# Optimization experiments

Hardware: AMD Instinct MI355X
Metric: run time of the kernel (lower is better)

Reference implementation:

```python
import jax, jax.numpy as jnp
import numpy as np

N_HEADS = 16
N_KV_HEADS = 4
HEAD_DIM = 128
WINDOW = 512
THETA = 10000.0


def _rotate_half(t):
    h = t.shape[-1] // 2
    return jnp.concatenate([-t[..., h:], t[..., :h]], axis=-1)


def setup_inputs() -> dict:
    key = jax.random.key(0)
    ks = jax.random.split(key, 6)
    B, S, D = 1, 2048, 2048
    sd = 1.0 / np.sqrt(D)
    x = jax.random.normal(ks[0], (B, S, D), dtype=jnp.float32)
    Wq = jax.random.normal(ks[1], (D, N_HEADS * HEAD_DIM), dtype=jnp.float32) * sd
    Wk = jax.random.normal(ks[2], (D, N_KV_HEADS * HEAD_DIM), dtype=jnp.float32) * sd
    Wv = jax.random.normal(ks[3], (D, N_KV_HEADS * HEAD_DIM), dtype=jnp.float32) * sd
    Wo = jax.random.normal(ks[4], (N_HEADS * HEAD_DIM, D), dtype=jnp.float32) * sd
    lam = jnp.full((N_HEADS,), 0.1, dtype=jnp.float32)
    return {"x": x, "Wq": Wq, "Wk": Wk, "Wv": Wv, "Wo": Wo, "lam": lam}


def reference(x, Wq, Wk, Wv, Wo, lam):
    B, S, D = x.shape
    H, Hk, hd = N_HEADS, N_KV_HEADS, HEAD_DIM
    n_rep = H // Hk

    q = (x @ Wq).reshape(B, S, H, hd).transpose(0, 2, 1, 3)   # [B,H,S,hd]
    k = (x @ Wk).reshape(B, S, Hk, hd).transpose(0, 2, 1, 3)  # [B,Hk,S,hd]
    v = (x @ Wv).reshape(B, S, Hk, hd).transpose(0, 2, 1, 3)

    # RoPE (full head_dim rotation, duplicated freqs)
    inv_freq = 1.0 / (THETA ** (jnp.arange(0, hd, 2, dtype=jnp.float32) / hd))
    t = jnp.arange(S, dtype=jnp.float32)
    freqs = jnp.outer(t, inv_freq)                 # [S, hd/2]
    emb = jnp.concatenate([freqs, freqs], axis=-1)  # [S, hd]
    cos, sin = jnp.cos(emb), jnp.sin(emb)
    q = q * cos + _rotate_half(q) * sin
    k = k * cos + _rotate_half(k) * sin

    # GQA: repeat KV heads
    k = jnp.repeat(k, n_rep, axis=1)  # [B,H,S,hd]
    v = jnp.repeat(v, n_rep, axis=1)

    sub = hd // 2
    q1, q2 = q[..., :sub], q[..., sub:]
    k1, k2 = k[..., :sub], k[..., sub:]
    scale = 1.0 / np.sqrt(sub)

    attn1 = jnp.einsum("bhqd,bhkd->bhqk", q1, k1) * scale
    attn2 = jnp.einsum("bhqd,bhkd->bhqk", q2, k2) * scale

    # causal + sliding window mask
    row = jnp.arange(S)[:, None]
    col = jnp.arange(S)[None, :]
    allowed = (col <= row) & (col >= row - WINDOW + 1)  # [S,S]
    neg_inf = jnp.float32(-jnp.inf)
    attn1 = jnp.where(allowed, attn1, neg_inf)
    attn2 = jnp.where(allowed, attn2, neg_inf)

    a1 = jax.nn.softmax(attn1.astype(jnp.float32), axis=-1).astype(x.dtype)
    a2 = jax.nn.softmax(attn2.astype(jnp.float32), axis=-1).astype(x.dtype)

    diff = jax.nn.relu(a1 - lam.reshape(1, H, 1, 1) * a2)
    diff = diff / (diff.sum(axis=-1, keepdims=True) + 1e-6)

    out = jnp.einsum("bhqk,bhkd->bhqd", diff, v)       # [B,H,S,hd]
    out = out.transpose(0, 2, 1, 3).reshape(B, S, H * hd)
    return out @ Wo
```

## Files before the change

### kernel.cpp

```cpp
#include <hip/hip_runtime.h>

typedef unsigned int u32;
typedef unsigned short u16;
typedef __attribute__((ext_vector_type(4))) float f32x4;
typedef __attribute__((ext_vector_type(8))) short s16x8;

#define S_LEN 2048
#define DMODEL 2048
#define NH 16
#define NKV 4
#define HD 128
#define WIN 512
#define QSCALE 0.18033688011112042f

#define WAIT_VMCNT4 asm volatile("s_waitcnt vmcnt(4)" ::: "memory")
#define WAIT_VMCNT0 asm volatile("s_waitcnt vmcnt(0)" ::: "memory")

__device__ __forceinline__ u16 f2bf(float f) {
  union { float f; u32 u; } v; v.f = f;
  u32 r = v.u + 0x7FFFu + ((v.u >> 16) & 1u);
  return (u16)(r >> 16);
}
__device__ __forceinline__ float bf2f(u16 h) {
  union { u32 u; float f; } v; v.u = ((u32)h) << 16;
  return v.f;
}

__device__ __forceinline__ void async16(const void* g, void* l) {
  __builtin_amdgcn_global_load_lds((const __attribute__((address_space(1))) void*)g,
                                   (__attribute__((address_space(3))) void*)l, 16, 0, 0);
}

__global__ __launch_bounds__(256) void k_prep(const float* __restrict__ x, u16* __restrict__ xb,
                                              const float* __restrict__ Wq,
                                              const float* __restrict__ Wk,
                                              const float* __restrict__ Wv,
                                              const float* __restrict__ Wo,
                                              u16* __restrict__ WT, u16* __restrict__ WoT,
                                              float2* __restrict__ cs) {
  __shared__ float tile[32][33];
  const int bid = blockIdx.x;
  if (bid >= 14336) {
    int s = (bid - 14336) * 4 + (threadIdx.x >> 6);
    int d = threadIdx.x & 63;
    float invf = expf(-((float)(2 * d) / (float)HD) * logf(10000.0f));
    float fr = (float)s * invf;
    float sv, cv;
    sincosf(fr, &sv, &cv);
    cs[s * 64 + d] = make_float2(cv, sv);
    return;
  }
  if (bid < 4096) {
    int i = bid * 256 + threadIdx.x;
    float4 v = ((const float4*)x)[i];
    ushort4 o;
    o.x = f2bf(v.x); o.y = f2bf(v.y); o.z = f2bf(v.z); o.w = f2bf(v.w);
    ((ushort4*)xb)[i] = o;
    return;
  }
  const int b = bid - 4096;
  const float* src;
  u16* dst;
  int N, nt, kt;
  if (b < 4096) {
    src = Wq; dst = WT; N = 2048; nt = b & 63; kt = b >> 6;
  } else if (b < 5120) {
    int i = b - 4096;
    src = Wk; dst = WT + (size_t)2048 * 2048; N = 512; nt = i & 15; kt = i >> 4;
  } else if (b < 6144) {
    int i = b - 5120;
    src = Wv; dst = WT + (size_t)2560 * 2048; N = 512; nt = i & 15; kt = i >> 4;
  } else {
    int i = b - 6144;
    src = Wo; dst = WoT; N = 2048; nt = i & 63; kt = i >> 6;
  }
  const int tx = threadIdx.x & 31, ty = threadIdx.x >> 5;
  const int n0 = nt * 32, k0 = kt * 32;
#pragma unroll
  for (int i = 0; i < 4; ++i)
    tile[ty + 8 * i][tx] = src[(size_t)(k0 + ty + 8 * i) * N + n0 + tx];
  __syncthreads();
#pragma unroll
  for (int i = 0; i < 4; ++i)
    dst[(size_t)(n0 + ty + 8 * i) * 2048 + k0 + tx] = f2bf(tile[tx][ty + 8 * i]);
}

__global__ void k_rope_k(u16* __restrict__ kr, const float2* __restrict__ cs) {
  int i = blockIdx.x * blockDim.x + threadIdx.x;
  int rowg = i >> 6, d = i & 63;
  int s = rowg & (S_LEN - 1);
  float2 c = cs[s * 64 + d];
  u16* p = kr + (size_t)rowg * HD;
  float a = bf2f(p[d]), b = bf2f(p[d + 64]);
  p[d]      = f2bf(a * c.x - b * c.y);
  p[d + 64] = f2bf(b * c.x + a * c.y);
}


template <int MODE>
__global__ __launch_bounds__(256) void k_gemm(const u16* __restrict__ A, const u16* __restrict__ BT,
                                              float* __restrict__ Cf, int K, int N,
                                              u16* __restrict__ qr, u16* __restrict__ kr,
                                              u16* __restrict__ vt) {
  __shared__ u16 S[2][192 * 64];
  const int t = threadIdx.x;
  const int l = t & 63, w = t >> 6;
  const int lg = l >> 4, ll = l & 15;

  const u32 nwg = gridDim.x * gridDim.y;
  const u32 bid = blockIdx.y * gridDim.x + blockIdx.x;
  const u32 sid = (bid & 7u) * (nwg >> 3) + (bid >> 3);
  const int m0 = (int)(sid % gridDim.x) * 64;
  const int n0 = (int)(sid / gridDim.x) * 128;

  const int wm = (w >> 1) * 32, wn = (w & 1) * 64;

  const u16* gp[6];
  u32 lo[6];
#pragma unroll
  for (int j = 0; j < 6; ++j) {
    u32 u = (u32)t * 16u + (u32)j * 4096u;
    u32 row = u >> 7;
    u32 slot = ((u >> 4) & 7u) ^ (row & 7u);
    lo[j] = u;
    gp[j] = (row < 64 ? A + (size_t)(m0 + (int)row) * K
                      : BT + (size_t)(n0 + (int)(row - 64)) * K) + slot * 8;
  }
  auto stage = [&](int b, int k0) {
#pragma unroll
    for (int j = 0; j < 6; ++j) async16(gp[j] + k0, (char*)S[b] + lo[j]);
  };

  f32x4 acc[2][4];
#pragma unroll
  for (int i = 0; i < 2; ++i)
#pragma unroll
    for (int j = 0; j < 4; ++j) acc[i][j] = (f32x4){0.f, 0.f, 0.f, 0.f};

  stage(0, 0);
  __syncthreads();

  const int nit = K / 64;
#pragma unroll 2
  for (int it = 0; it < nit; ++it) {
    const int cur = it & 1;
    if (it + 1 < nit) stage(cur ^ 1, (it + 1) * 64);

    s16x8 af[2][2], bq[4][2];
#pragma unroll
    for (int mt = 0; mt < 2; ++mt) {
      u32 r = (u32)(wm + mt * 16 + ll);
#pragma unroll
      for (int ks = 0; ks < 2; ++ks)
        af[mt][ks] = *(const s16x8*)((const char*)S[cur] + r * 128u +
                                     ((((u32)(ks * 4 + lg)) ^ (r & 7u)) * 16u));
    }
#pragma unroll
    for (int nt = 0; nt < 4; ++nt) {
      u32 r = (u32)(64 + wn + nt * 16 + ll);
#pragma unroll
      for (int ks = 0; ks < 2; ++ks)
        bq[nt][ks] = *(const s16x8*)((const char*)S[cur] + r * 128u +
                                     ((((u32)(ks * 4 + lg)) ^ (r & 7u)) * 16u));
    }
#pragma unroll
    for (int ks = 0; ks < 2; ++ks)
#pragma unroll
      for (int mt = 0; mt < 2; ++mt)
#pragma unroll
        for (int nt = 0; nt < 4; ++nt)
          acc[mt][nt] = __builtin_amdgcn_mfma_f32_16x16x32_bf16(af[mt][ks], bq[nt][ks],
                                                                acc[mt][nt], 0, 0, 0);
    __syncthreads();
  }

  if (MODE == 1) {
#pragma unroll
    for (int mt = 0; mt < 2; ++mt) {
      int srow = m0 + wm + mt * 16 + lg * 4;
#pragma unroll
      for (int nt = 0; nt < 4; ++nt) {
        int col = n0 + wn + nt * 16 + ll;
        f32x4 a = acc[mt][nt];
#pragma unroll
        for (int j = 0; j < 4; ++j) Cf[(size_t)(srow + j) * N + col] = a[j];
      }
    }
  } else {
#pragma unroll
    for (int nt = 0; nt < 4; ++nt) {
      int cb = n0 + wn + nt * 16;
#pragma unroll
      for (int mt = 0; mt < 2; ++mt) {
        int srow = m0 + wm + mt * 16 + lg * 4;
        f32x4 a = acc[mt][nt];
        if (cb < 2048) {
          int hh = cb >> 7, d = (cb & 127) + ll;
          u16* p = qr + ((size_t)hh * S_LEN) * HD + d;
#pragma unroll
          for (int j = 0; j < 4; ++j) p[(size_t)(srow + j) * HD] = f2bf(a[j]);
        } else if (cb < 2560) {
          int hh = (cb - 2048) >> 7, d = ((cb - 2048) & 127) + ll;
          u16* p = kr + ((size_t)hh * S_LEN) * HD + d;
#pragma unroll
          for (int j = 0; j < 4; ++j) p[(size_t)(srow + j) * HD] = f2bf(a[j]);
        } else {
          int hh = (cb - 2560) >> 7, d = ((cb - 2560) & 127) + ll;
          ushort4 pk;
          pk.x = f2bf(a[0]); pk.y = f2bf(a[1]); pk.z = f2bf(a[2]); pk.w = f2bf(a[3]);
          *(ushort4*)(vt + ((size_t)hh * HD + d) * S_LEN + srow) = pk;
        }
      }
    }
  }
}

__global__ __launch_bounds__(256, 3) void k_attn(const u16* __restrict__ qr,
                                                 const u16* __restrict__ kr,
                                                 const u16* __restrict__ vt,
                                                 const float* __restrict__ lam,
                                                 const float2* __restrict__ cs,
                                                 u16* __restrict__ ao) {
  __shared__ u16 KV[3][8192];
  __shared__ u16 P[4][16 * 40];
  const int t = threadIdx.x;
  const int l = t & 63, w = t >> 6;
  const int lg = l >> 4, ll = l & 15;
  const int hkv = blockIdx.y;
  const int h = hkv * 4 + w;
  const int qs = blockIdx.x * 16;
  const int row = qs + ll;

  const u16* Qp = qr + ((size_t)h * S_LEN + qs) * HD;
  const u16* Kp = kr + (size_t)hkv * S_LEN * HD;
  const u16* Vp = vt + (size_t)hkv * HD * S_LEN;

  const int kbeg = (qs >= 512) ? ((qs - 511) & ~63) : 0;
  const int nch1 = (qs + 15 - kbeg) / 64 + 1;
  const int nch2 = (qs + 15 - kbeg) / 32 + 1;

  u32 ku1[4], kr1[4], ks1[4];
#pragma unroll
  for (int j = 0; j < 4; ++j) {
    u32 u = (u32)t * 16u + (u32)j * 4096u;
    ku1[j] = u;
    kr1[j] = u >> 8;
    ks1[j] = ((u >> 4) & 15u) ^ (kr1[j] & 7u);
  }
  u32 ku2[2], kr2[2], ks2[2], vu2[2], vd2[2], vk2[2];
#pragma unroll
  for (int j = 0; j < 2; ++j) {
    u32 u = (u32)t * 16u + (u32)j * 4096u;
    ku2[j] = u;
    kr2[j] = u >> 8;
    ks2[j] = ((u >> 4) & 15u) ^ (kr2[j] & 7u);
    u32 r = u >> 7;
    u32 lgc = ((u >> 4) & 7u) ^ (r & 7u);
    vu2[j] = u;
    vd2[j] = 2u * r + (lgc >> 2);
    vk2[j] = (lgc & 3u) * 8u;
  }

  auto stage1 = [&](int buf, int tcc) {
    const int c = kbeg + tcc * 64;
    char* dst = (char*)KV + (size_t)buf * 16384;
#pragma unroll
    for (int j = 0; j < 4; ++j)
      async16(Kp + (size_t)(c + kr1[j]) * HD + ks1[j] * 8, dst + ku1[j]);
  };
  auto stage2 = [&](int buf, int tcc) {
    const int c = kbeg + tcc * 32;
    char* dst = (char*)KV + (size_t)buf * 16384;
#pragma unroll
    for (int j = 0; j < 2; ++j) {
      async16(Kp + (size_t)(c + kr2[j]) * HD + ks2[j] * 8, dst + ku2[j]);
      async16(Vp + (size_t)vd2[j] * S_LEN + c + vk2[j], dst + 8192 + vu2[j]);
    }
  };

  s16x8 qa[4];
#pragma unroll
  for (int i = 0; i < 4; ++i)
    qa[i] = *(const s16x8*)(Qp + (size_t)ll * HD + i * 32 + lg * 8);
  {
    const float4* cp4 = (const float4*)(cs + (size_t)row * 64);
#pragma unroll
    for (int i = 0; i < 2; ++i) {
      float4 cv[4];
#pragma unroll
      for (int jj = 0; jj < 4; ++jj) cv[jj] = cp4[i * 16 + lg * 4 + jj];
      s16x8 lo = qa[i], hi = qa[i + 2];
#pragma unroll
      for (int j = 0; j < 8; ++j) {
        float cc = (j & 1) ? cv[j >> 1].z : cv[j >> 1].x;
        float ss = (j & 1) ? cv[j >> 1].w : cv[j >> 1].y;
        float a = bf2f((u16)lo[j]), b = bf2f((u16)hi[j]);
        lo[j] = (short)f2bf((a * cc - b * ss) * QSCALE);
        hi[j] = (short)f2bf((b * cc + a * ss) * QSCALE);
      }
      qa[i] = lo; qa[i + 2] = hi;
    }
  }

  const f32x4 zero = {0.f, 0.f, 0.f, 0.f};
  float z1 = 0.f, z2 = 0.f;

  stage1(0, 0);
  stage1(1, (nch1 > 1) ? 1 : 0);

  for (int tc = 0; tc < nch1; ++tc) {
    WAIT_VMCNT4;
    __builtin_amdgcn_s_barrier();
    {
      int ci = tc + 2; if (ci > nch1 - 1) ci = nch1 - 1;
      stage1((tc + 2) % 3, ci);
    }
    const int c = kbeg + tc * 64;
    const u16* Kb = (const u16*)((const char*)KV + (size_t)(tc % 3) * 16384);
    float acc1 = 0.f, acc2 = 0.f;
#pragma unroll
    for (int kt = 0; kt < 4; ++kt) {
      const int kbase = c + kt * 16;
      if (kbase > qs + 15 || kbase + 15 < qs - (WIN - 1)) continue;
      const int kr_ = kt * 16 + ll;
      const u16* kp = Kb + kr_ * 128;
      const u32 sw = (u32)(kr_ & 7);
      s16x8 b0 = *(const s16x8*)(kp + ((lg ^ sw) * 8));
      s16x8 b1 = *(const s16x8*)(kp + (((4 + lg) ^ sw) * 8));
      s16x8 b2 = *(const s16x8*)(kp + (((8 + lg) ^ sw) * 8));
      s16x8 b3 = *(const s16x8*)(kp + (((12 + lg) ^ sw) * 8));
      f32x4 a = __builtin_amdgcn_mfma_f32_16x16x32_bf16(b0, qa[0], zero, 0, 0, 0);
      a = __builtin_amdgcn_mfma_f32_16x16x32_bf16(b1, qa[1], a, 0, 0, 0);
      f32x4 b = __builtin_amdgcn_mfma_f32_16x16x32_bf16(b2, qa[2], zero, 0, 0, 0);
      b = __builtin_amdgcn_mfma_f32_16x16x32_bf16(b3, qa[3], b, 0, 0, 0);
      const bool fullk = (kbase + 15 <= qs) && (kbase >= qs - 496);
      if (!fullk) {
#pragma unroll
        for (int j = 0; j < 4; ++j) {
          int key = kbase + lg * 4 + j;
          bool ok = (key <= row) && (key > row - WIN);
          a[j] = ok ? a[j] : -1e30f;
          b[j] = ok ? b[j] : -1e30f;
        }
      }
#pragma unroll
      for (int j = 0; j < 4; ++j) {
        acc1 += __builtin_amdgcn_exp2f(a[j]);
        acc2 += __builtin_amdgcn_exp2f(b[j]);
      }
    }
    z1 += acc1; z2 += acc2;
  }

  z1 += __shfl_xor(z1, 16, 64); z1 += __shfl_xor(z1, 32, 64);
  z2 += __shfl_xor(z2, 16, 64); z2 += __shfl_xor(z2, 32, 64);
  const float l2z1 = __builtin_amdgcn_logf(z1);
  const float l2z2 = __builtin_amdgcn_logf(z2);
  const float lm = lam[h];

  f32x4 o[8];
#pragma unroll
  for (int dt = 0; dt < 8; ++dt) o[dt] = zero;
  float dsum = 0.f;
  u16* Pw = &P[w][0];

  WAIT_VMCNT0;
  __syncthreads();

  stage2(0, 0);
  stage2(1, (nch2 > 1) ? 1 : 0);

  for (int tc = 0; tc < nch2; ++tc) {
    WAIT_VMCNT4;
    __builtin_amdgcn_s_barrier();
    {
      int ci = tc + 2; if (ci > nch2 - 1) ci = nch2 - 1;
      stage2((tc + 2) % 3, ci);
    }
    const int c = kbeg + tc * 32;
    const u16* Kb = (const u16*)((const char*)KV + (size_t)(tc % 3) * 16384);
    const u16* Vb = Kb + 4096;
    const bool full = (c + 31 <= qs) && (c >= qs - 496);
    __builtin_amdgcn_s_setprio(1);
#pragma unroll
    for (int kt = 0; kt < 2; ++kt) {
      const int kr_ = kt * 16 + ll;
      const u16* kp = Kb + kr_ * 128;
      const u32 sw = (u32)(kr_ & 7);
      s16x8 b0 = *(const s16x8*)(kp + ((lg ^ sw) * 8));
      s16x8 b1 = *(const s16x8*)(kp + (((4 + lg) ^ sw) * 8));
      s16x8 b2 = *(const s16x8*)(kp + (((8 + lg) ^ sw) * 8));
      s16x8 b3 = *(const s16x8*)(kp + (((12 + lg) ^ sw) * 8));
      f32x4 a = __builtin_amdgcn_mfma_f32_16x16x32_bf16(b0, qa[0], zero, 0, 0, 0);
      a = __builtin_amdgcn_mfma_f32_16x16x32_bf16(b1, qa[1], a, 0, 0, 0);
      f32x4 b = __builtin_amdgcn_mfma_f32_16x16x32_bf16(b2, qa[2], zero, 0, 0, 0);
      b = __builtin_amdgcn_mfma_f32_16x16x32_bf16(b3, qa[3], b, 0, 0, 0);
      if (!full) {
#pragma unroll
        for (int j = 0; j < 4; ++j) {
          int key = c + kt * 16 + lg * 4 + j;
          bool ok = (key <= row) && (key > row - WIN);
          a[j] = ok ? a[j] : -1e30f;
          b[j] = ok ? b[j] : -1e30f;
        }
      }
      float d4[4];
#pragma unroll
      for (int j = 0; j < 4; ++j) {
        float a1 = __builtin_amdgcn_exp2f(a[j] - l2z1);
        float a2 = __builtin_amdgcn_exp2f(b[j] - l2z2);
        float d = fmaxf(fmaf(-lm, a2, a1), 0.f);
        d4[j] = d;
        dsum += d;
      }
      u32 p01, p23;
      asm("v_cvt_pk_bf16_f32 %0, %1, %2" : "=v"(p01) : "v"(d4[0]), "v"(d4[1]));
      asm("v_cvt_pk_bf16_f32 %0, %1, %2" : "=v"(p23) : "v"(d4[2]), "v"(d4[3]));
      uint2 pk; pk.x = p01; pk.y = p23;
      *(uint2*)(&Pw[ll * 40 + kt * 16 + lg * 4]) = pk;
    }
    s16x8 pf = *(const s16x8*)(&Pw[ll * 40 + lg * 8]);
#pragma unroll
    for (int dt = 0; dt < 8; ++dt) {
      const int d = dt * 16 + ll;
      const u32 r = (u32)(d >> 1);
      const u32 phys = ((u32)((d & 1) * 4 + lg)) ^ (r & 7u);
      s16x8 vf = *(const s16x8*)(Vb + r * 64 + phys * 8);
      o[dt] = __builtin_amdgcn_mfma_f32_16x16x32_bf16(pf, vf, o[dt], 0, 0, 0);
    }
    __builtin_amdgcn_s_setprio(0);
  }
  WAIT_VMCNT0;

  dsum += __shfl_xor(dsum, 16, 64);
  dsum += __shfl_xor(dsum, 32, 64);
  const float rds = __builtin_amdgcn_rcpf(dsum + 1e-6f);
  float rdsj[4];
#pragma unroll
  for (int j = 0; j < 4; ++j) rdsj[j] = __shfl(rds, lg * 4 + j, 64);

#pragma unroll
  for (int dt = 0; dt < 8; ++dt) {
#pragma unroll
    for (int j = 0; j < 4; ++j) {
      int srow = qs + lg * 4 + j;
      ao[(size_t)srow * DMODEL + h * HD + dt * 16 + ll] = f2bf(o[dt][j] * rdsj[j]);
    }
  }
}


extern "C" void kernel_launch(void* const* d_in, const int* in_sizes, int n_in,
                              void* d_out, int out_size, void* d_ws, size_t ws_size,
                              hipStream_t stream) {
  const float* x = (const float*)d_in[0];
  const float* Wq = (const float*)d_in[1];
  const float* Wk = (const float*)d_in[2];
  const float* Wv = (const float*)d_in[3];
  const float* Wo = (const float*)d_in[4];
  const float* lam = (const float*)d_in[5];
  float* out = (float*)d_out;

  char* ws = (char*)d_ws;
  u16* xb = (u16*)(ws);
  u16* WT = (u16*)(ws + (8u << 20));
  u16* WoT = (u16*)(ws + (20u << 20));
  u16* qr = (u16*)(ws + (28u << 20));
  u16* kr = (u16*)(ws + (36u << 20));
  u16* vt = (u16*)(ws + (38u << 20));
  u16* ao = (u16*)(ws + (40u << 20));
  float2* cs = (float2*)(ws + (48u << 20));

  k_prep<<<14848, 256, 0, stream>>>(x, xb, Wq, Wk, Wv, Wo, WT, WoT, cs);

  k_gemm<0><<<dim3(32, 24), 256, 0, stream>>>(xb, WT, nullptr, 2048, 3072, qr, kr, vt);

  k_rope_k<<<(NKV * S_LEN * 64) / 256, 256, 0, stream>>>(kr, cs);

  k_attn<<<dim3(S_LEN / 16, NKV), 256, 0, stream>>>(qr, kr, vt, lam, cs, ao);

  k_gemm<1><<<dim3(32, 16), 256, 0, stream>>>(ao, WoT, out, 2048, 2048, nullptr, nullptr, nullptr);
}
```

Baseline: 115.6 us.

## Switch GEMM to triple-buffered K=32 async LDS pipeline with single barrier

```diff
diff --git a/kernel.cpp b/kernel.cpp
--- a/kernel.cpp
+++ b/kernel.cpp
@@ -14,6 +14,7 @@
 #define QSCALE 0.18033688011112042f
 
 #define WAIT_VMCNT4 asm volatile("s_waitcnt vmcnt(4)" ::: "memory")
+#define WAIT_VMCNT3 asm volatile("s_waitcnt vmcnt(3)" ::: "memory")
 #define WAIT_VMCNT0 asm volatile("s_waitcnt vmcnt(0)" ::: "memory")
 
 __device__ __forceinline__ u16 f2bf(float f) {
@@ -98,11 +99,11 @@
 
 
 template <int MODE>
-__global__ __launch_bounds__(256) void k_gemm(const u16* __restrict__ A, const u16* __restrict__ BT,
-                                              float* __restrict__ Cf, int K, int N,
-                                              u16* __restrict__ qr, u16* __restrict__ kr,
-                                              u16* __restrict__ vt) {
-  __shared__ u16 S[2][192 * 64];
+__global__ __launch_bounds__(256, 4) void k_gemm(const u16* __restrict__ A, const u16* __restrict__ BT,
+                                                 float* __restrict__ Cf, int K, int N,
+                                                 u16* __restrict__ qr, u16* __restrict__ kr,
+                                                 u16* __restrict__ vt) {
+  __shared__ u16 S[3][192 * 32];
   const int t = threadIdx.x;
   const int l = t & 63, w = t >> 6;
   const int lg = l >> 4, ll = l & 15;
@@ -115,20 +116,21 @@
 
   const int wm = (w >> 1) * 32, wn = (w & 1) * 64;
 
-  const u16* gp[6];
-  u32 lo[6];
-#pragma unroll
-  for (int j = 0; j < 6; ++j) {
+  const u16* gp[3];
+  u32 lo[3];
+#pragma unroll
+  for (int j = 0; j < 3; ++j) {
     u32 u = (u32)t * 16u + (u32)j * 4096u;
-    u32 row = u >> 7;
-    u32 slot = ((u >> 4) & 7u) ^ (row & 7u);
+    u32 row = u >> 6;
+    u32 slot = (u >> 4) & 3u;
+    u32 kb = (slot ^ ((row ^ (row >> 2)) & 3u)) * 8u;
     lo[j] = u;
     gp[j] = (row < 64 ? A + (size_t)(m0 + (int)row) * K
-                      : BT + (size_t)(n0 + (int)(row - 64)) * K) + slot * 8;
-  }
-  auto stage = [&](int b, int k0) {
-#pragma unroll
-    for (int j = 0; j < 6; ++j) async16(gp[j] + k0, (char*)S[b] + lo[j]);
+                      : BT + (size_t)(n0 + (int)(row - 64)) * K) + kb;
+  }
+  auto stage = [&](int buf, int k0) {
+#pragma unroll
+    for (int j = 0; j < 3; ++j) async16(gp[j] + k0, (char*)S[buf] + lo[j]);
   };
 
   f32x4 acc[2][4];
@@ -137,41 +139,32 @@
 #pragma unroll
     for (int j = 0; j < 4; ++j) acc[i][j] = (f32x4){0.f, 0.f, 0.f, 0.f};
 
+  const int nit = K / 32;
   stage(0, 0);
-  __syncthreads();
-
-  const int nit = K / 64;
-#pragma unroll 2
+  stage(1, 32);
+
   for (int it = 0; it < nit; ++it) {
-    const int cur = it & 1;
-    if (it + 1 < nit) stage(cur ^ 1, (it + 1) * 64);
-
-    s16x8 af[2][2], bq[4][2];
+    if (it < nit - 1) { WAIT_VMCNT3; } else { WAIT_VMCNT0; }
+    __builtin_amdgcn_s_barrier();
+    if (it + 2 < nit) stage((it + 2) % 3, (it + 2) * 32);
+
+    const char* Sb = (const char*)S[it % 3];
+    s16x8 af[2], bq[4];
 #pragma unroll
     for (int mt = 0; mt < 2; ++mt) {
       u32 r = (u32)(wm + mt * 16 + ll);
-#pragma unroll
-      for (int ks = 0; ks < 2; ++ks)
-        af[mt][ks] = *(const s16x8*)((const char*)S[cur] + r * 128u +
-                                     ((((u32)(ks * 4 + lg)) ^ (r & 7u)) * 16u));
+      af[mt] = *(const s16x8*)(Sb + r * 64u + ((lg ^ ((r ^ (r >> 2)) & 3u)) * 16u));
     }
 #pragma unroll
     for (int nt = 0; nt < 4; ++nt) {
       u32 r = (u32)(64 + wn + nt * 16 + ll);
-#pragma unroll
-      for (int ks = 0; ks < 2; ++ks)
-        bq[nt][ks] = *(const s16x8*)((const char*)S[cur] + r * 128u +
-                                     ((((u32)(ks * 4 + lg)) ^ (r & 7u)) * 16u));
-    }
-#pragma unroll
-    for (int ks = 0; ks < 2; ++ks)
-#pragma unroll
-      for (int mt = 0; mt < 2; ++mt)
-#pragma unroll
-        for (int nt = 0; nt < 4; ++nt)
-          acc[mt][nt] = __builtin_amdgcn_mfma_f32_16x16x32_bf16(af[mt][ks], bq[nt][ks],
-                                                                acc[mt][nt], 0, 0, 0);
-    __syncthreads();
+      bq[nt] = *(const s16x8*)(Sb + r * 64u + ((lg ^ ((r ^ (r >> 2)) & 3u)) * 16u));
+    }
+#pragma unroll
+    for (int mt = 0; mt < 2; ++mt)
+#pragma unroll
+      for (int nt = 0; nt < 4; ++nt)
+        acc[mt][nt] = __builtin_amdgcn_mfma_f32_16x16x32_bf16(af[mt], bq[nt], acc[mt][nt], 0, 0, 0);
   }
 
   if (MODE == 1) {
```

After: 130.6 us. 13.0% more time.

## Split softmax normalizer pass into separate key-split kernel

Applied to the files above, without the earlier changes.

```diff
diff --git a/kernel.cpp b/kernel.cpp
--- a/kernel.cpp
+++ b/kernel.cpp
@@ -11,6 +11,7 @@
 #define NKV 4
 #define HD 128
 #define WIN 512
+#define ZSPL 2
 #define QSCALE 0.18033688011112042f
 
 #define WAIT_VMCNT4 asm volatile("s_waitcnt vmcnt(4)" ::: "memory")
@@ -215,11 +216,128 @@
   }
 }
 
+__global__ __launch_bounds__(256, 4) void k_attn_z(const u16* __restrict__ qr,
+                                                   const u16* __restrict__ kr,
+                                                   const float2* __restrict__ cs,
+                                                   float2* __restrict__ zp) {
+  __shared__ u16 KB[2][8192];
+  const int t = threadIdx.x;
+  const int l = t & 63, w = t >> 6;
+  const int lg = l >> 4, ll = l & 15;
+  const int hkv = blockIdx.y;
+  const int spl = blockIdx.z;
+  const int h = hkv * 4 + w;
+  const int qs = blockIdx.x * 16;
+  const int row = qs + ll;
+
+  const int kbeg = (qs >= 512) ? ((qs - 511) & ~63) : 0;
+  const int nch = (qs + 15 - kbeg) / 64 + 1;
+  const int per = (nch + ZSPL - 1) / ZSPL;
+  const int c0 = spl * per;
+  const int c1 = (nch < c0 + per) ? nch : (c0 + per);
+
+  float z1 = 0.f, z2 = 0.f;
+
+  if (c0 < c1) {
+    const u16* Qp = qr + ((size_t)h * S_LEN + qs) * HD;
+    const u16* Kp = kr + (size_t)hkv * S_LEN * HD;
+
+    u32 ku1[4], kr1[4], ks1[4];
+#pragma unroll
+    for (int j = 0; j < 4; ++j) {
+      u32 u = (u32)t * 16u + (u32)j * 4096u;
+      ku1[j] = u;
+      kr1[j] = u >> 8;
+      ks1[j] = ((u >> 4) & 15u) ^ (kr1[j] & 7u);
+    }
+    auto stageZ = [&](int buf, int tcc) {
+      const int c = kbeg + tcc * 64;
+      char* dst = (char*)KB + (size_t)buf * 16384;
+#pragma unroll
+      for (int j = 0; j < 4; ++j)
+        async16(Kp + (size_t)(c + kr1[j]) * HD + ks1[j] * 8, dst + ku1[j]);
+    };
+
+    s16x8 qa[4];
+#pragma unroll
+    for (int i = 0; i < 4; ++i)
+      qa[i] = *(const s16x8*)(Qp + (size_t)ll * HD + i * 32 + lg * 8);
+    {
+      const float4* cp4 = (const float4*)(cs + (size_t)row * 64);
+#pragma unroll
+      for (int i = 0; i < 2; ++i) {
+        float4 cv[4];
+#pragma unroll
+        for (int jj = 0; jj < 4; ++jj) cv[jj] = cp4[i * 16 + lg * 4 + jj];
+        s16x8 lo = qa[i], hi = qa[i + 2];
+#pragma unroll
+        for (int j = 0; j < 8; ++j) {
+          float cc = (j & 1) ? cv[j >> 1].z : cv[j >> 1].x;
+          float ss = (j & 1) ? cv[j >> 1].w : cv[j >> 1].y;
+          float a = bf2f((u16)lo[j]), b = bf2f((u16)hi[j]);
+          lo[j] = (short)f2bf((a * cc - b * ss) * QSCALE);
+          hi[j] = (short)f2bf((b * cc + a * ss) * QSCALE);
+        }
+        qa[i] = lo; qa[i + 2] = hi;
+      }
+    }
+
+    const f32x4 zero = {0.f, 0.f, 0.f, 0.f};
+    stageZ(0, c0);
+
+    for (int tc = c0; tc < c1; ++tc) {
+      __syncthreads();
+      if (tc + 1 < c1) stageZ((tc + 1) & 1, tc + 1);
+      const int c = kbeg + tc * 64;
+      const u16* Kb = (const u16*)((const char*)KB + (size_t)(tc & 1) * 16384);
+      float acc1 = 0.f, acc2 = 0.f;
+#pragma unroll
+      for (int kt = 0; kt < 4; ++kt) {
+        const int kbase = c + kt * 16;
+        if (kbase > qs + 15 || kbase + 15 < qs - (WIN - 1)) continue;
+        const int kr_ = kt * 16 + ll;
+        const u16* kp = Kb + kr_ * 128;
+        const u32 sw = (u32)(kr_ & 7);
+        s16x8 b0 = *(const s16x8*)(kp + ((lg ^ sw) * 8));
+        s16x8 b1 = *(const s16x8*)(kp + (((4 + lg) ^ sw) * 8));
+        s16x8 b2 = *(const s16x8*)(kp + (((8 + lg) ^ sw) * 8));
+        s16x8 b3 = *(const s16x8*)(kp + (((12 + lg) ^ sw) * 8));
+        f32x4 a = __builtin_amdgcn_mfma_f32_16x16x32_bf16(b0, qa[0], zero, 0, 0, 0);
+        a = __builtin_amdgcn_mfma_f32_16x16x32_bf16(b1, qa[1], a, 0, 0, 0);
+        f32x4 b = __builtin_amdgcn_mfma_f32_16x16x32_bf16(b2, qa[2], zero, 0, 0, 0);
+        b = __builtin_amdgcn_mfma_f32_16x16x32_bf16(b3, qa[3], b, 0, 0, 0);
+        const bool fullk = (kbase + 15 <= qs) && (kbase >= qs - 496);
+        if (!fullk) {
+#pragma unroll
+          for (int j = 0; j < 4; ++j) {
+            int key = kbase + lg * 4 + j;
+            bool ok = (key <= row) && (key > row - WIN);
+            a[j] = ok ? a[j] : -1e30f;
+            b[j] = ok ? b[j] : -1e30f;
+          }
+        }
+#pragma unroll
+        for (int j = 0; j < 4; ++j) {
+          acc1 += __builtin_amdgcn_exp2f(a[j]);
+          acc2 += __builtin_amdgcn_exp2f(b[j]);
+        }
+      }
+      z1 += acc1; z2 += acc2;
+    }
+  }
+
+  z1 += __shfl_xor(z1, 16, 64); z1 += __shfl_xor(z1, 32, 64);
+  z2 += __shfl_xor(z2, 16, 64); z2 += __shfl_xor(z2, 32, 64);
+  if (lg == 0)
+    zp[((size_t)spl * NH + h) * S_LEN + row] = make_float2(z1, z2);
+}
+
 __global__ __launch_bounds__(256, 3) void k_attn(const u16* __restrict__ qr,
                                                  const u16* __restrict__ kr,
                                                  const u16* __restrict__ vt,
                                                  const float* __restrict__ lam,
                                                  const float2* __restrict__ cs,
+                                                 const float2* __restrict__ zp,
                                                  u16* __restrict__ ao) {
   __shared__ u16 KV[3][8192];
   __shared__ u16 P[4][16 * 40];
@@ -236,17 +354,8 @@
   const u16* Vp = vt + (size_t)hkv * HD * S_LEN;
 
   const int kbeg = (qs >= 512) ? ((qs - 511) & ~63) : 0;
-  const int nch1 = (qs + 15 - kbeg) / 64 + 1;
   const int nch2 = (qs + 15 - kbeg) / 32 + 1;
 
-  u32 ku1[4], kr1[4], ks1[4];
-#pragma unroll
-  for (int j = 0; j < 4; ++j) {
-    u32 u = (u32)t * 16u + (u32)j * 4096u;
-    ku1[j] = u;
-    kr1[j] = u >> 8;
-    ks1[j] = ((u >> 4) & 15u) ^ (kr1[j] & 7u);
-  }
   u32 ku2[2], kr2[2], ks2[2], vu2[2], vd2[2], vk2[2];
 #pragma unroll
   for (int j = 0; j < 2; ++j) {
@@ -260,14 +369,6 @@
     vd2[j] = 2u * r + (lgc >> 2);
     vk2[j] = (lgc & 3u) * 8u;
   }
-
-  auto stage1 = [&](int buf, int tcc) {
-    const int c = kbeg + tcc * 64;
-    char* dst = (char*)KV + (size_t)buf * 16384;
-#pragma unroll
-    for (int j = 0; j < 4; ++j)
-      async16(Kp + (size_t)(c + kr1[j]) * HD + ks1[j] * 8, dst + ku1[j]);
-  };
   auto stage2 = [&](int buf, int tcc) {
     const int c = kbeg + tcc * 32;
     char* dst = (char*)KV + (size_t)buf * 16384;
@@ -277,6 +378,9 @@
       async16(Vp + (size_t)vd2[j] * S_LEN + c + vk2[j], dst + 8192 + vu2[j]);
     }
   };
+
+  stage2(0, 0);
+  stage2(1, (nch2 > 1) ? 1 : 0);
 
   s16x8 qa[4];
 #pragma unroll
@@ -301,74 +405,22 @@
       qa[i] = lo; qa[i + 2] = hi;
     }
   }
-
-  const f32x4 zero = {0.f, 0.f, 0.f, 0.f};
   float z1 = 0.f, z2 = 0.f;
-
-  stage1(0, 0);
-  stage1(1, (nch1 > 1) ? 1 : 0);
-
-  for (int tc = 0; tc < nch1; ++tc) {
-    WAIT_VMCNT4;
-    __builtin_amdgcn_s_barrier();
-    {
-      int ci = tc + 2; if (ci > nch1 - 1) ci = nch1 - 1;
-      stage1((tc + 2) % 3, ci);
-    }
-    const int c = kbeg + tc * 64;
-    const u16* Kb = (const u16*)((const char*)KV + (size_t)(tc % 3) * 16384);
-    float acc1 = 0.f, acc2 = 0.f;
-#pragma unroll
-    for (int kt = 0; kt < 4; ++kt) {
-      const int kbase = c + kt * 16;
-      if (kbase > qs + 15 || kbase + 15 < qs - (WIN - 1)) continue;
-      const int kr_ = kt * 16 + ll;
-      const u16* kp = Kb + kr_ * 128;
-      const u32 sw = (u32)(kr_ & 7);
-      s16x8 b0 = *(const s16x8*)(kp + ((lg ^ sw) * 8));
-      s16x8 b1 = *(const s16x8*)(kp + (((4 + lg) ^ sw) * 8));
-      s16x8 b2 = *(const s16x8*)(kp + (((8 + lg) ^ sw) * 8));
-      s16x8 b3 = *(const s16x8*)(kp + (((12 + lg) ^ sw) * 8));
-      f32x4 a = __builtin_amdgcn_mfma_f32_16x16x32_bf16(b0, qa[0], zero, 0, 0, 0);
-      a = __builtin_amdgcn_mfma_f32_16x16x32_bf16(b1, qa[1], a, 0, 0, 0);
-      f32x4 b = __builtin_amdgcn_mfma_f32_16x16x32_bf16(b2, qa[2], zero, 0, 0, 0);
-      b = __builtin_amdgcn_mfma_f32_16x16x32_bf16(b3, qa[3], b, 0, 0, 0);
-      const bool fullk = (kbase + 15 <= qs) && (kbase >= qs - 496);
-      if (!fullk) {
-#pragma unroll
-        for (int j = 0; j < 4; ++j) {
-          int key = kbase + lg * 4 + j;
-          bool ok = (key <= row) && (key > row - WIN);
-          a[j] = ok ? a[j] : -1e30f;
-          b[j] = ok ? b[j] : -1e30f;
-        }
-      }
-#pragma unroll
-      for (int j = 0; j < 4; ++j) {
-        acc1 += __builtin_amdgcn_exp2f(a[j]);
-        acc2 += __builtin_amdgcn_exp2f(b[j]);
-      }
-    }
-    z1 += acc1; z2 += acc2;
-  }
-
-  z1 += __shfl_xor(z1, 16, 64); z1 += __shfl_xor(z1, 32, 64);
-  z2 += __shfl_xor(z2, 16, 64); z2 += __shfl_xor(z2, 32, 64);
+#pragma unroll
+  for (int s = 0; s < ZSPL; ++s) {
+    float2 zz = zp[((size_t)s * NH + h) * S_LEN + row];
+    z1 += zz.x; z2 += zz.y;
+  }
   const float l2z1 = __builtin_amdgcn_logf(z1);
   const float l2z2 = __builtin_amdgcn_logf(z2);
   const float lm = lam[h];
 
+  const f32x4 zero = {0.f, 0.f, 0.f, 0.f};
   f32x4 o[8];
 #pragma unroll
   for (int dt = 0; dt < 8; ++dt) o[dt] = zero;
   float dsum = 0.f;
   u16* Pw = &P[w][0];
-
-  WAIT_VMCNT0;
-  __syncthreads();
-
-  stage2(0, 0);
-  stage2(1, (nch2 > 1) ? 1 : 0);
 
   for (int tc = 0; tc < nch2; ++tc) {
     WAIT_VMCNT4;
@@ -470,6 +522,7 @@
   u16* vt = (u16*)(ws + (38u << 20));
   u16* ao = (u16*)(ws + (40u << 20));
   float2* cs = (float2*)(ws + (48u << 20));
+  float2* zp = (float2*)(ws + (49u << 20));
 
   k_prep<<<14848, 256, 0, stream>>>(x, xb, Wq, Wk, Wv, Wo, WT, WoT, cs);
 
@@ -477,7 +530,8 @@
 
   k_rope_k<<<(NKV * S_LEN * 64) / 256, 256, 0, stream>>>(kr, cs);
 
-  k_attn<<<dim3(S_LEN / 16, NKV), 256, 0, stream>>>(qr, kr, vt, lam, cs, ao);
+  k_attn_z<<<dim3(S_LEN / 16, NKV, ZSPL), 256, 0, stream>>>(qr, kr, cs, zp);
+  k_attn<<<dim3(S_LEN / 16, NKV), 256, 0, stream>>>(qr, kr, vt, lam, cs, zp, ao);
 
   k_gemm<1><<<dim3(32, 16), 256, 0, stream>>>(ao, WoT, out, 2048, 2048, nullptr, nullptr, nullptr);
 }
```

Measured after the change: 120.2 us. 4.0% more time.

## Load V directly from global into registers, use 64-key chunks in pass two

Applied to the files above, without the earlier changes.

```diff
diff --git a/kernel.cpp b/kernel.cpp
--- a/kernel.cpp
+++ b/kernel.cpp
@@ -215,14 +215,14 @@
   }
 }
 
-__global__ __launch_bounds__(256, 3) void k_attn(const u16* __restrict__ qr,
+__global__ __launch_bounds__(256, 2) void k_attn(const u16* __restrict__ qr,
                                                  const u16* __restrict__ kr,
                                                  const u16* __restrict__ vt,
                                                  const float* __restrict__ lam,
                                                  const float2* __restrict__ cs,
                                                  u16* __restrict__ ao) {
   __shared__ u16 KV[3][8192];
-  __shared__ u16 P[4][16 * 40];
+  __shared__ u16 P[4][16 * 72];
   const int t = threadIdx.x;
   const int l = t & 63, w = t >> 6;
   const int lg = l >> 4, ll = l & 15;
@@ -236,8 +236,7 @@
   const u16* Vp = vt + (size_t)hkv * HD * S_LEN;
 
   const int kbeg = (qs >= 512) ? ((qs - 511) & ~63) : 0;
-  const int nch1 = (qs + 15 - kbeg) / 64 + 1;
-  const int nch2 = (qs + 15 - kbeg) / 32 + 1;
+  const int nch = (qs + 15 - kbeg) / 64 + 1;
 
   u32 ku1[4], kr1[4], ks1[4];
 #pragma unroll
@@ -247,35 +246,12 @@
     kr1[j] = u >> 8;
     ks1[j] = ((u >> 4) & 15u) ^ (kr1[j] & 7u);
   }
-  u32 ku2[2], kr2[2], ks2[2], vu2[2], vd2[2], vk2[2];
-#pragma unroll
-  for (int j = 0; j < 2; ++j) {
-    u32 u = (u32)t * 16u + (u32)j * 4096u;
-    ku2[j] = u;
-    kr2[j] = u >> 8;
-    ks2[j] = ((u >> 4) & 15u) ^ (kr2[j] & 7u);
-    u32 r = u >> 7;
-    u32 lgc = ((u >> 4) & 7u) ^ (r & 7u);
-    vu2[j] = u;
-    vd2[j] = 2u * r + (lgc >> 2);
-    vk2[j] = (lgc & 3u) * 8u;
-  }
-
-  auto stage1 = [&](int buf, int tcc) {
+  auto stageK = [&](int buf, int tcc) {
     const int c = kbeg + tcc * 64;
     char* dst = (char*)KV + (size_t)buf * 16384;
 #pragma unroll
     for (int j = 0; j < 4; ++j)
       async16(Kp + (size_t)(c + kr1[j]) * HD + ks1[j] * 8, dst + ku1[j]);
-  };
-  auto stage2 = [&](int buf, int tcc) {
-    const int c = kbeg + tcc * 32;
-    char* dst = (char*)KV + (size_t)buf * 16384;
-#pragma unroll
-    for (int j = 0; j < 2; ++j) {
-      async16(Kp + (size_t)(c + kr2[j]) * HD + ks2[j] * 8, dst + ku2[j]);
-      async16(Vp + (size_t)vd2[j] * S_LEN + c + vk2[j], dst + 8192 + vu2[j]);
-    }
   };
 
   s16x8 qa[4];
@@ -305,15 +281,15 @@
   const f32x4 zero = {0.f, 0.f, 0.f, 0.f};
   float z1 = 0.f, z2 = 0.f;
 
-  stage1(0, 0);
-  stage1(1, (nch1 > 1) ? 1 : 0);
-
-  for (int tc = 0; tc < nch1; ++tc) {
+  stageK(0, 0);
+  stageK(1, (nch > 1) ? 1 : 0);
+
+  for (int tc = 0; tc < nch; ++tc) {
     WAIT_VMCNT4;
     __builtin_amdgcn_s_barrier();
     {
-      int ci = tc + 2; if (ci > nch1 - 1) ci = nch1 - 1;
-      stage1((tc + 2) % 3, ci);
+      int ci = tc + 2; if (ci > nch - 1) ci = nch - 1;
+      stageK((tc + 2) % 3, ci);
     }
     const int c = kbeg + tc * 64;
     const u16* Kb = (const u16*)((const char*)KV + (size_t)(tc % 3) * 16384);
@@ -367,23 +343,36 @@
   WAIT_VMCNT0;
   __syncthreads();
 
-  stage2(0, 0);
-  stage2(1, (nch2 > 1) ? 1 : 0);
-
-  for (int tc = 0; tc < nch2; ++tc) {
+  stageK(0, 0);
+  stageK(1, (nch > 1) ? 1 : 0);
+
+  for (int tc = 0; tc < nch; ++tc) {
     WAIT_VMCNT4;
     __builtin_amdgcn_s_barrier();
+    const int c = kbeg + tc * 64;
+
+    s16x8 vf[8][2];
+#pragma unroll
+    for (int dt = 0; dt < 8; ++dt) {
+      const u16* vp = Vp + (size_t)(dt * 16 + ll) * S_LEN + c + lg * 8;
+      vf[dt][0] = *(const s16x8*)(vp);
+      vf[dt][1] = *(const s16x8*)(vp + 32);
+    }
     {
-      int ci = tc + 2; if (ci > nch2 - 1) ci = nch2 - 1;
-      stage2((tc + 2) % 3, ci);
-    }
-    const int c = kbeg + tc * 32;
+      int ci = tc + 2; if (ci > nch - 1) ci = nch - 1;
+      stageK((tc + 2) % 3, ci);
+    }
+
     const u16* Kb = (const u16*)((const char*)KV + (size_t)(tc % 3) * 16384);
-    const u16* Vb = Kb + 4096;
-    const bool full = (c + 31 <= qs) && (c >= qs - 496);
     __builtin_amdgcn_s_setprio(1);
 #pragma unroll
-    for (int kt = 0; kt < 2; ++kt) {
+    for (int kt = 0; kt < 4; ++kt) {
+      const int kbase = c + kt * 16;
+      if (kbase > qs + 15 || kbase + 15 < qs - (WIN - 1)) {
+        ushort4 zz; zz.x = zz.y = zz.z = zz.w = 0;
+        *(ushort4*)(&Pw[ll * 72 + kt * 16 + lg * 4]) = zz;
+        continue;
+      }
       const int kr_ = kt * 16 + ll;
       const u16* kp = Kb + kr_ * 128;
       const u32 sw = (u32)(kr_ & 7);
@@ -395,10 +384,11 @@
       a = __builtin_amdgcn_mfma_f32_16x16x32_bf16(b1, qa[1], a, 0, 0, 0);
       f32x4 b = __builtin_amdgcn_mfma_f32_16x16x32_bf16(b2, qa[2], zero, 0, 0, 0);
       b = __builtin_amdgcn_mfma_f32_16x16x32_bf16(b3, qa[3], b, 0, 0, 0);
-      if (!full) {
+      const bool fullk = (kbase + 15 <= qs) && (kbase >= qs - 496);
+      if (!fullk) {
 #pragma unroll
         for (int j = 0; j < 4; ++j) {
-          int key = c + kt * 16 + lg * 4 + j;
+          int key = kbase + lg * 4 + j;
           bool ok = (key <= row) && (key > row - WIN);
           a[j] = ok ? a[j] : -1e30f;
           b[j] = ok ? b[j] : -1e30f;
@@ -417,16 +407,14 @@
       asm("v_cvt_pk_bf16_f32 %0, %1, %2" : "=v"(p01) : "v"(d4[0]), "v"(d4[1]));
       asm("v_cvt_pk_bf16_f32 %0, %1, %2" : "=v"(p23) : "v"(d4[2]), "v"(d4[3]));
       uint2 pk; pk.x = p01; pk.y = p23;
-      *(uint2*)(&Pw[ll * 40 + kt * 16 + lg * 4]) = pk;
-    }
-    s16x8 pf = *(const s16x8*)(&Pw[ll * 40 + lg * 8]);
+      *(uint2*)(&Pw[ll * 72 + kt * 16 + lg * 4]) = pk;
+    }
+    s16x8 pf0 = *(const s16x8*)(&Pw[ll * 72 + lg * 8]);
+    s16x8 pf1 = *(const s16x8*)(&Pw[ll * 72 + 32 + lg * 8]);
 #pragma unroll
     for (int dt = 0; dt < 8; ++dt) {
-      const int d = dt * 16 + ll;
-      const u32 r = (u32)(d >> 1);
-      const u32 phys = ((u32)((d & 1) * 4 + lg)) ^ (r & 7u);
-      s16x8 vf = *(const s16x8*)(Vb + r * 64 + phys * 8);
-      o[dt] = __builtin_amdgcn_mfma_f32_16x16x32_bf16(pf, vf, o[dt], 0, 0, 0);
+      o[dt] = __builtin_amdgcn_mfma_f32_16x16x32_bf16(pf0, vf[dt][0], o[dt], 0, 0, 0);
+      o[dt] = __builtin_amdgcn_mfma_f32_16x16x32_bf16(pf1, vf[dt][1], o[dt], 0, 0, 0);
     }
     __builtin_amdgcn_s_setprio(0);
   }
```

Result: slower. 132.7 us (+14.8%).
